# Optimization experiments

Measured on AMD Instinct MI355X. Metric: run time of the kernel, lower is better.

## Reference

```python
import jax, jax.numpy as jnp
import numpy as np

MARGIN = 0.3


def setup_inputs() -> dict:
    key = jax.random.key(0)
    k1, k2 = jax.random.split(key)
    N, D, C = 8192, 512, 1024
    embeddings = jax.random.normal(k1, (N, D), dtype=jnp.float32)
    labels = jax.random.randint(k2, (N,), 0, C, dtype=jnp.int64)
    return {"embeddings": embeddings, "labels": labels}


def reference(embeddings, labels):
    # L2-normalize rows, cosine distance via Gram matrix: d = 1 - e_i . e_j
    e = embeddings / jnp.linalg.norm(embeddings, axis=1, keepdims=True)
    dist = 1.0 - jnp.matmul(e, e.T)  # [N, N]

    same = labels[:, None] == labels[None, :]           # [N, N] bool
    eye = jnp.eye(labels.shape[0], dtype=bool)
    pos_mask = same & ~eye                              # positives exclude self
    neg_mask = ~same                                    # negatives

    # Batch-hard mining: hardest (farthest) positive, hardest (closest) negative
    hardest_pos = jnp.max(jnp.where(pos_mask, dist, -jnp.inf), axis=1)
    hardest_neg = jnp.min(jnp.where(neg_mask, dist, jnp.inf), axis=1)

    loss = jax.nn.relu(hardest_pos - hardest_neg + MARGIN)
    return jnp.mean(loss)
```

## Files before the change

kernel.cpp:

```cpp
#include <hip/hip_runtime.h>
#include <hip/hip_fp8.h>
#include <hip/hip_fp16.h>
#include <stdint.h>

#define MARGIN 0.3f

constexpr int N = 8192;
constexpr int D = 512;
constexpr int BM = 128, BN = 128;
constexpr int NKB = D / 32;
constexpr int NT = N / BM;
constexpr int NPAIR = NT * (NT + 1) / 2;
constexpr int WEDGE = NPAIR / 8;
constexpr float ESCALE = 16.0f;
constexpr float INV_SC2 = 1.0f / (ESCALE * ESCALE);

typedef float f32x4 __attribute__((ext_vector_type(4)));

__device__ __forceinline__ unsigned char f2fp8(float f) {
  return __hip_fp8_e4m3(f).__x;
}

__device__ __forceinline__ unsigned packMM(float mn, float mx) {
  unsigned short a = __half_as_ushort(__float2half(mn));
  unsigned short b = __half_as_ushort(__float2half(mx));
  return (unsigned)a | ((unsigned)b << 16);
}
__device__ __forceinline__ float unpLo(unsigned u) {
  return __half2float(__ushort_as_half((unsigned short)(u & 0xffff)));
}
__device__ __forceinline__ float unpHi(unsigned u) {
  return __half2float(__ushort_as_half((unsigned short)(u >> 16)));
}
__device__ __forceinline__ unsigned combMM(unsigned A, unsigned B) {
  return packMM(fminf(unpLo(A), unpLo(B)), fmaxf(unpHi(A), unpHi(B)));
}

__device__ __forceinline__ void pair_from_q(int q, int& ti, int& tj) {
  int SI = 0;
  while (32 * (SI + 1) * (SI + 1) + 4 * (SI + 1) <= q) ++SI;
  int r = q - (32 * SI * SI + 4 * SI);
  int i, j, SJ;
  if (r < 64 * SI) {
    SJ = r >> 6;
    int w = r & 63;
    i = w >> 3;
    j = w & 7;
  } else {
    int d = r - 64 * SI;
    SJ = SI;
    i = 0;
    while ((i + 1) * (i + 2) / 2 <= d) ++i;
    j = d - i * (i + 1) / 2;
  }
  ti = SI * 8 + i;
  tj = SJ * 8 + j;
}


__global__ __launch_bounds__(256) void normalize_rows(
    const float* __restrict__ emb, unsigned char* __restrict__ e8) {
  const int wave = threadIdx.x >> 6, lane = threadIdx.x & 63;
  const int row = blockIdx.x * 4 + wave;
  const float4* src = (const float4*)(emb + (size_t)row * D);
  float4 x0 = src[lane];
  float4 x1 = src[lane + 64];
  float ss = x0.x * x0.x + x0.y * x0.y + x0.z * x0.z + x0.w * x0.w +
             x1.x * x1.x + x1.y * x1.y + x1.z * x1.z + x1.w * x1.w;
#pragma unroll
  for (int m = 1; m < 64; m <<= 1) ss += __shfl_xor(ss, m, 64);
  const float r = rsqrtf(ss) * ESCALE;
  union { unsigned char b[8]; uint2 u; } o;
  o.b[0] = f2fp8(x0.x * r); o.b[1] = f2fp8(x0.y * r);
  o.b[2] = f2fp8(x0.z * r); o.b[3] = f2fp8(x0.w * r);
  o.b[4] = f2fp8(x1.x * r); o.b[5] = f2fp8(x1.y * r);
  o.b[6] = f2fp8(x1.z * r); o.b[7] = f2fp8(x1.w * r);
  const unsigned off = (unsigned)(row >> 4) * 8192 + (unsigned)(lane >> 2) * 512 +
                       (row & 15) * 32 + (lane & 3) * 8;
  *(uint2*)(e8 + off) = o.u;
}

__global__ __launch_bounds__(256, 3) void bh_gemm_sym(
    const unsigned char* __restrict__ e8, const int* __restrict__ labels,
    unsigned* __restrict__ scr) {
  __shared__ unsigned bufR[2][128];
  __shared__ unsigned bufC[2][128];

  const int b = blockIdx.x;
  const int q = WEDGE * (b & 7) + (b >> 3);
  int ti, tj;
  pair_from_q(q, ti, tj);
  const int iBase = ti * BM, jBase = tj * BN;
  const bool diag = (ti == tj);

  const int tid = threadIdx.x;
  const int lane = tid & 63;
  const int wave = tid >> 6;
  const int wr = wave >> 1, wc = wave & 1;
  const int quad = lane >> 4, n16 = lane & 15;

  const unsigned laneOff = (unsigned)n16 * 32 + (unsigned)quad * 8;
  const unsigned char* aP[4];
  const unsigned char* bP[4];
#pragma unroll
  for (int r = 0; r < 4; ++r) {
    aP[r] = e8 + (unsigned)(iBase + wr * 64 + r * 16) * 512 + laneOff;
    bP[r] = e8 + (unsigned)(jBase + wc * 64 + r * 16) * 512 + laneOff;
  }

  f32x4 acc[4][4];
#pragma unroll
  for (int r = 0; r < 4; ++r)
#pragma unroll
    for (int c = 0; c < 4; ++c) acc[r][c] = (f32x4)0.0f;

  long abuf[3][4], bbuf[3][4];
#pragma unroll
  for (int r = 0; r < 4; ++r) {
    abuf[0][r] = *(const long*)(aP[r]);
    bbuf[0][r] = *(const long*)(bP[r]);
    abuf[1][r] = *(const long*)(aP[r] + 512);
    bbuf[1][r] = *(const long*)(bP[r] + 512);
  }

#pragma unroll
  for (int kb = 0; kb < NKB; ++kb) {
    const int cur = kb % 3;
    if (kb + 2 < NKB) {
      const int nxt = (kb + 2) % 3;
#pragma unroll
      for (int r = 0; r < 4; ++r) {
        abuf[nxt][r] = *(const long*)(aP[r] + (kb + 2) * 512);
        bbuf[nxt][r] = *(const long*)(bP[r] + (kb + 2) * 512);
      }
    }
#pragma unroll
    for (int r = 0; r < 4; ++r)
#pragma unroll
      for (int c = 0; c < 4; ++c)
        acc[r][c] = __builtin_amdgcn_mfma_f32_16x16x32_fp8_fp8(
            abuf[cur][r], bbuf[cur][c], acc[r][c], 0, 0, 0);
  }

  int lj[4];
#pragma unroll
  for (int c = 0; c < 4; ++c) lj[c] = labels[jBase + wc * 64 + c * 16 + n16];

  float cminp[4], cmaxn[4];
#pragma unroll
  for (int c = 0; c < 4; ++c) {
    cminp[c] = __builtin_inff();
    cmaxn[c] = -__builtin_inff();
  }

#pragma unroll
  for (int r = 0; r < 4; ++r) {
    const int rbase = wr * 64 + r * 16 + quad * 4;
    int4 li = *(const int4*)(labels + iBase + rbase);
    const int* lav = (const int*)&li;
    float minp[4], maxn[4];
#pragma unroll
    for (int v = 0; v < 4; ++v) {
      minp[v] = __builtin_inff();
      maxn[v] = -__builtin_inff();
    }
#pragma unroll
    for (int c = 0; c < 4; ++c) {
      const int col_ = wc * 64 + c * 16 + n16;
#pragma unroll
      for (int v = 0; v < 4; ++v) {
        float s = acc[r][c][v] * INV_SC2;
        bool same = (lav[v] == lj[c]);
        float pv = same ? s : __builtin_inff();
        float nv = same ? -__builtin_inff() : s;
        if (diag && (rbase + v) == col_) pv = __builtin_inff();
        minp[v] = fminf(minp[v], pv);
        maxn[v] = fmaxf(maxn[v], nv);
        cminp[c] = fminf(cminp[c], same ? s : __builtin_inff());
        cmaxn[c] = fmaxf(cmaxn[c], same ? -__builtin_inff() : s);
      }
    }
#pragma unroll
    for (int m = 1; m <= 8; m <<= 1) {
#pragma unroll
      for (int v = 0; v < 4; ++v) {
        minp[v] = fminf(minp[v], __shfl_xor(minp[v], m, 64));
        maxn[v] = fmaxf(maxn[v], __shfl_xor(maxn[v], m, 64));
      }
    }
    if (n16 == 0) {
#pragma unroll
      for (int v = 0; v < 4; ++v)
        bufR[wc][rbase + v] = packMM(minp[v], maxn[v]);
    }
  }

  if (!diag) {
#pragma unroll
    for (int m = 16; m <= 32; m <<= 1) {
#pragma unroll
      for (int c = 0; c < 4; ++c) {
        cminp[c] = fminf(cminp[c], __shfl_xor(cminp[c], m, 64));
        cmaxn[c] = fmaxf(cmaxn[c], __shfl_xor(cmaxn[c], m, 64));
      }
    }
    if (quad == 0) {
#pragma unroll
      for (int c = 0; c < 4; ++c)
        bufC[wr][wc * 64 + c * 16 + n16] = packMM(cminp[c], cmaxn[c]);
    }
  }

  __syncthreads();

  if (wc == 0) {
    const int row = wr * 64 + lane;
    scr[(unsigned)(iBase + row) * 64 + tj] = combMM(bufR[0][row], bufR[1][row]);
  }
  if (!diag && wr == 0) {
    const int col = wc * 64 + lane;
    scr[(unsigned)(jBase + col) * 64 + ti] = combMM(bufC[0][col], bufC[1][col]);
  }
}

__global__ __launch_bounds__(256) void finalize_loss(
    const unsigned* __restrict__ scr, float* __restrict__ out) {
  const int row = blockIdx.x * 256 + threadIdx.x;
  const uint4* p = (const uint4*)(scr + (unsigned)row * 64);
  float mn = __builtin_inff(), mx = -__builtin_inff();
#pragma unroll
  for (int i = 0; i < 16; ++i) {
    uint4 w = p[i];
    mn = fminf(fminf(fminf(mn, unpLo(w.x)), unpLo(w.y)), fminf(unpLo(w.z), unpLo(w.w)));
    mx = fmaxf(fmaxf(fmaxf(mx, unpHi(w.x)), unpHi(w.y)), fmaxf(unpHi(w.z), unpHi(w.w)));
  }
  float loss = mx - mn + MARGIN;
  float sum = loss > 0.f ? loss : 0.f;
#pragma unroll
  for (int m = 1; m < 64; m <<= 1) sum += __shfl_xor(sum, m, 64);
  __shared__ float ws4[4];
  const int lane = threadIdx.x & 63, wave = threadIdx.x >> 6;
  if (lane == 0) ws4[wave] = sum;
  __syncthreads();
  if (threadIdx.x == 0)
    atomicAdd(out, (ws4[0] + ws4[1] + ws4[2] + ws4[3]) * (1.0f / N));
}

extern "C" void kernel_launch(void* const* d_in, const int* in_sizes, int n_in,
                              void* d_out, int out_size, void* d_ws, size_t ws_size,
                              hipStream_t stream) {
  const float* emb = (const float*)d_in[0];
  const int* labels = (const int*)d_in[1];
  float* out = (float*)d_out;

  unsigned char* e8 = (unsigned char*)d_ws;
  unsigned* scr = (unsigned*)((char*)d_ws + (size_t)4 * 1024 * 1024);

  hipMemsetAsync(out, 0, sizeof(float), stream);
  normalize_rows<<<N / 4, 256, 0, stream>>>(emb, e8);
  bh_gemm_sym<<<NPAIR, 256, 0, stream>>>(e8, labels, scr);
  finalize_loss<<<N / 256, 256, 0, stream>>>(scr, out);
}
```

Baseline: 116.3 us.

## Shrink symmetric GEMM tiles to 64x64 single-wave blocks without shared memory

```diff
diff --git a/kernel.cpp b/kernel.cpp
--- a/kernel.cpp
+++ b/kernel.cpp
@@ -7,9 +7,9 @@
 
 constexpr int N = 8192;
 constexpr int D = 512;
-constexpr int BM = 128, BN = 128;
+constexpr int BT = 64;
 constexpr int NKB = D / 32;
-constexpr int NT = N / BM;
+constexpr int NT = N / BT;
 constexpr int NPAIR = NT * (NT + 1) / 2;
 constexpr int WEDGE = NPAIR / 8;
 constexpr float ESCALE = 16.0f;
@@ -32,29 +32,26 @@
 __device__ __forceinline__ float unpHi(unsigned u) {
   return __half2float(__ushort_as_half((unsigned short)(u >> 16)));
 }
-__device__ __forceinline__ unsigned combMM(unsigned A, unsigned B) {
-  return packMM(fminf(unpLo(A), unpLo(B)), fmaxf(unpHi(A), unpHi(B)));
-}
 
 __device__ __forceinline__ void pair_from_q(int q, int& ti, int& tj) {
   int SI = 0;
-  while (32 * (SI + 1) * (SI + 1) + 4 * (SI + 1) <= q) ++SI;
-  int r = q - (32 * SI * SI + 4 * SI);
+  while (128 * (SI + 1) * (SI + 1) + 8 * (SI + 1) <= q) ++SI;
+  int r = q - (128 * SI * SI + 8 * SI);
   int i, j, SJ;
-  if (r < 64 * SI) {
-    SJ = r >> 6;
-    int w = r & 63;
-    i = w >> 3;
-    j = w & 7;
+  if (r < 256 * SI) {
+    SJ = r >> 8;
+    int w = r & 255;
+    i = w >> 4;
+    j = w & 15;
   } else {
-    int d = r - 64 * SI;
+    int d = r - 256 * SI;
     SJ = SI;
     i = 0;
     while ((i + 1) * (i + 2) / 2 <= d) ++i;
     j = d - i * (i + 1) / 2;
   }
-  ti = SI * 8 + i;
-  tj = SJ * 8 + j;
+  ti = SI * 16 + i;
+  tj = SJ * 16 + j;
 }
 
 
@@ -80,32 +77,26 @@
   *(uint2*)(e8 + off) = o.u;
 }
 
-__global__ __launch_bounds__(256, 3) void bh_gemm_sym(
+__global__ __launch_bounds__(64, 4) void bh_gemm_sym(
     const unsigned char* __restrict__ e8, const int* __restrict__ labels,
     unsigned* __restrict__ scr) {
-  __shared__ unsigned bufR[2][128];
-  __shared__ unsigned bufC[2][128];
-
   const int b = blockIdx.x;
   const int q = WEDGE * (b & 7) + (b >> 3);
   int ti, tj;
   pair_from_q(q, ti, tj);
-  const int iBase = ti * BM, jBase = tj * BN;
+  const int iBase = ti * BT, jBase = tj * BT;
   const bool diag = (ti == tj);
 
-  const int tid = threadIdx.x;
-  const int lane = tid & 63;
-  const int wave = tid >> 6;
-  const int wr = wave >> 1, wc = wave & 1;
+  const int lane = threadIdx.x;
   const int quad = lane >> 4, n16 = lane & 15;
-
   const unsigned laneOff = (unsigned)n16 * 32 + (unsigned)quad * 8;
+
   const unsigned char* aP[4];
   const unsigned char* bP[4];
 #pragma unroll
   for (int r = 0; r < 4; ++r) {
-    aP[r] = e8 + (unsigned)(iBase + wr * 64 + r * 16) * 512 + laneOff;
-    bP[r] = e8 + (unsigned)(jBase + wc * 64 + r * 16) * 512 + laneOff;
+    aP[r] = e8 + (unsigned)(iBase + r * 16) * 512 + laneOff;
+    bP[r] = e8 + (unsigned)(jBase + r * 16) * 512 + laneOff;
   }
 
   f32x4 acc[4][4];
@@ -116,12 +107,12 @@
 
   long abuf[3][4], bbuf[3][4];
 #pragma unroll
-  for (int r = 0; r < 4; ++r) {
-    abuf[0][r] = *(const long*)(aP[r]);
-    bbuf[0][r] = *(const long*)(bP[r]);
-    abuf[1][r] = *(const long*)(aP[r] + 512);
-    bbuf[1][r] = *(const long*)(bP[r] + 512);
-  }
+  for (int ph = 0; ph < 2; ++ph)
+#pragma unroll
+    for (int r = 0; r < 4; ++r) {
+      abuf[ph][r] = *(const long*)(aP[r] + ph * 512);
+      bbuf[ph][r] = *(const long*)(bP[r] + ph * 512);
+    }
 
 #pragma unroll
   for (int kb = 0; kb < NKB; ++kb) {
@@ -144,7 +135,7 @@
 
   int lj[4];
 #pragma unroll
-  for (int c = 0; c < 4; ++c) lj[c] = labels[jBase + wc * 64 + c * 16 + n16];
+  for (int c = 0; c < 4; ++c) lj[c] = labels[jBase + c * 16 + n16];
 
   float cminp[4], cmaxn[4];
 #pragma unroll
@@ -155,7 +146,7 @@
 
 #pragma unroll
   for (int r = 0; r < 4; ++r) {
-    const int rbase = wr * 64 + r * 16 + quad * 4;
+    const int rbase = r * 16 + quad * 4;
     int4 li = *(const int4*)(labels + iBase + rbase);
     const int* lav = (const int*)&li;
     float minp[4], maxn[4];
@@ -166,7 +157,7 @@
     }
 #pragma unroll
     for (int c = 0; c < 4; ++c) {
-      const int col_ = wc * 64 + c * 16 + n16;
+      const int col_ = c * 16 + n16;
 #pragma unroll
       for (int v = 0; v < 4; ++v) {
         float s = acc[r][c][v] * INV_SC2;
@@ -191,7 +182,7 @@
     if (n16 == 0) {
 #pragma unroll
       for (int v = 0; v < 4; ++v)
-        bufR[wc][rbase + v] = packMM(minp[v], maxn[v]);
+        scr[(unsigned)(iBase + rbase + v) * 128 + tj] = packMM(minp[v], maxn[v]);
     }
   }
 
@@ -207,29 +198,18 @@
     if (quad == 0) {
 #pragma unroll
       for (int c = 0; c < 4; ++c)
-        bufC[wr][wc * 64 + c * 16 + n16] = packMM(cminp[c], cmaxn[c]);
-    }
-  }
-
-  __syncthreads();
-
-  if (wc == 0) {
-    const int row = wr * 64 + lane;
-    scr[(unsigned)(iBase + row) * 64 + tj] = combMM(bufR[0][row], bufR[1][row]);
-  }
-  if (!diag && wr == 0) {
-    const int col = wc * 64 + lane;
-    scr[(unsigned)(jBase + col) * 64 + ti] = combMM(bufC[0][col], bufC[1][col]);
+        scr[(unsigned)(jBase + c * 16 + n16) * 128 + ti] = packMM(cminp[c], cmaxn[c]);
+    }
   }
 }
 
 __global__ __launch_bounds__(256) void finalize_loss(
     const unsigned* __restrict__ scr, float* __restrict__ out) {
   const int row = blockIdx.x * 256 + threadIdx.x;
-  const uint4* p = (const uint4*)(scr + (unsigned)row * 64);
+  const uint4* p = (const uint4*)(scr + (size_t)row * 128);
   float mn = __builtin_inff(), mx = -__builtin_inff();
 #pragma unroll
-  for (int i = 0; i < 16; ++i) {
+  for (int i = 0; i < 32; ++i) {
     uint4 w = p[i];
     mn = fminf(fminf(fminf(mn, unpLo(w.x)), unpLo(w.y)), fminf(unpLo(w.z), unpLo(w.w)));
     mx = fmaxf(fmaxf(fmaxf(mx, unpHi(w.x)), unpHi(w.y)), fmaxf(unpHi(w.z), unpHi(w.w)));
@@ -258,6 +238,6 @@
 
   hipMemsetAsync(out, 0, sizeof(float), stream);
   normalize_rows<<<N / 4, 256, 0, stream>>>(emb, e8);
-  bh_gemm_sym<<<NPAIR, 256, 0, stream>>>(e8, labels, scr);
+  bh_gemm_sym<<<NPAIR, 64, 0, stream>>>(e8, labels, scr);
   finalize_loss<<<N / 256, 256, 0, stream>>>(scr, out);
 }
```

Result: slower. 137.3 us (+18.1%).
